# Performance work log

Hardware: AMD Instinct MI355X
Metric: run time of the kernel (lower is better)

Reference implementation:

```python
import jax, jax.numpy as jnp
import numpy as np
import math

B, S, D = 4, 2048, 1024

def setup_inputs() -> dict:
    key = jax.random.key(0)
    ks = jax.random.split(key, 8)
    scale = 1.0 / math.sqrt(D)
    x = jax.random.normal(ks[0], (B, S, D), dtype=jnp.float32)
    # additive causal mask: 0 on/below diag, -1e9 above (broadcast over batch)
    causal = jnp.where(jnp.tril(jnp.ones((S, S), dtype=bool)), 0.0, -1e9).astype(jnp.float32)
    mask = jnp.broadcast_to(causal, (B, S, S))
    Wq = jax.random.uniform(ks[1], (D, D), jnp.float32, -scale, scale)
    bq = jax.random.uniform(ks[2], (D,), jnp.float32, -scale, scale)
    Wk = jax.random.uniform(ks[3], (D, D), jnp.float32, -scale, scale)
    bk = jax.random.uniform(ks[4], (D,), jnp.float32, -scale, scale)
    Wv = jax.random.uniform(ks[5], (D, D), jnp.float32, -scale, scale)
    bv = jax.random.uniform(ks[6], (D,), jnp.float32, -scale, scale)
    return {"x": x, "mask": mask, "Wq": Wq, "bq": bq, "Wk": Wk, "bk": bk, "Wv": Wv, "bv": bv}

def reference(x, mask, Wq, bq, Wk, bk, Wv, bv):
    q = jnp.einsum('bsd,de->bse', x, Wq) + bq
    k = jnp.einsum('bsd,de->bse', x, Wk) + bk
    v = jnp.einsum('bsd,de->bse', x, Wv) + bv
    scores = jnp.einsum('bqd,bkd->bqk', q, k) / math.sqrt(k.shape[-1])
    attn = jax.nn.softmax(scores + mask, axis=-1)
    return jnp.einsum('bqk,bkd->bqd', attn, v)
```

## Files before the change

kernel.cpp:

```cpp
#include <hip/hip_runtime.h>
#include <hip/hip_bf16.h>
#include <math.h>

typedef short v8s __attribute__((ext_vector_type(8)));
typedef short v4s __attribute__((ext_vector_type(4)));
typedef float v4f __attribute__((ext_vector_type(4)));
typedef unsigned short ushort_t;

__device__ __forceinline__ unsigned short f2bf(float f) {
    unsigned int u = __float_as_uint(f);
    u = (u + 0x7FFFu + ((u >> 16) & 1u)) >> 16;
    return (unsigned short)u;
}

__device__ __forceinline__ void load_lds16(const void* g, void* l) {
    __builtin_amdgcn_global_load_lds((const __attribute__((address_space(1))) void*)g,
                                     (__attribute__((address_space(3))) void*)l,
                                     16, 0, 0);
}

#define FENCE() asm volatile("" ::: "memory")
#define BAR() do { FENCE(); __builtin_amdgcn_s_barrier(); FENCE(); } while (0)

__global__ __launch_bounds__(256) void cvt_kernel(const float4* __restrict__ in,
                                                  ushort_t* __restrict__ out, int n4) {
    int i = blockIdx.x * 256 + threadIdx.x;
    int stride = gridDim.x * 256;
    for (; i < n4; i += stride) {
        float4 v = in[i];
        v4s p;
        p[0] = (short)f2bf(v.x); p[1] = (short)f2bf(v.y);
        p[2] = (short)f2bf(v.z); p[3] = (short)f2bf(v.w);
        *(v4s*)(out + (size_t)i * 4) = p;
    }
}

__global__ void transpose_w(const float* __restrict__ W0, const float* __restrict__ W1,
                            const float* __restrict__ W2, ushort_t* __restrict__ WtAll) {
    const float* W = (blockIdx.z == 0) ? W0 : (blockIdx.z == 1 ? W1 : W2);
    ushort_t* out = WtAll + (size_t)blockIdx.z * 1024 * 1024;
    __shared__ float tile[32][33];
    int n0 = blockIdx.x * 32, k0 = blockIdx.y * 32;
    int tx = threadIdx.x, ty = threadIdx.y;
    #pragma unroll
    for (int i = 0; i < 32; i += 8)
        tile[ty + i][tx] = W[(size_t)(k0 + ty + i) * 1024 + n0 + tx];
    __syncthreads();
    #pragma unroll
    for (int i = 0; i < 32; i += 8)
        out[(size_t)(n0 + ty + i) * 1024 + k0 + tx] = f2bf(tile[tx][ty + i]);
}

template <int MODE>
__global__ __launch_bounds__(MODE == 3 ? 256 : 512)
void gemm_ring(const ushort_t* __restrict__ A, int lda, long long strideA,
               const ushort_t* __restrict__ Bt, int ldb, long long strideB,
               const float* __restrict__ bq, const float* __restrict__ bk,
               const float* __restrict__ bv,
               ushort_t* __restrict__ Qb, ushort_t* __restrict__ Kb,
               ushort_t* __restrict__ Vt,
               float* __restrict__ Cf, int ldc, long long strideC, int K)
{
    constexpr int THREADS = (MODE == 3) ? 256 : 512;
    constexpr int BN      = (MODE == 3) ? 128 : 256;
    constexpr int NW      = THREADS / 64;
    constexpr int RPL     = THREADS / 4;
    constexpr int ALINES  = 128 / RPL;
    constexpr int BLINES  = BN / RPL;

    int bx, by, bz = 0;
    int f = blockIdx.x;
    if constexpr (MODE == 0) {
        int xcd = f & 7, i = f >> 3;
        by = xcd * 8 + i / 12;
        bx = i % 12;
    } else if constexpr (MODE == 2) {
        int swz = (f & 7) * 36 + (f >> 3);
        bz = swz / 72; int t = swz % 72;
        int r = 0, c = 0;
        while (c + (r / 2 + 1) <= t) { c += r / 2 + 1; ++r; }
        by = r; bx = t - c;
    } else {
        int swz = (f & 7) * 64 + (f >> 3);
        bz = swz >> 7; int rem = swz & 127;
        by = 15 - (rem >> 3); bx = rem & 7;
    }

    const int tid = threadIdx.x;
    const int lane = tid & 63, wid = tid >> 6;
    const int wm = (NW == 8) ? (wid >> 2) : (wid >> 1);
    const int wc = wid & ((NW == 8) ? 3 : 1);

    const ushort_t* Ab = A + (size_t)bz * strideA;
    const ushort_t* Bb = Bt + (size_t)bz * strideB;

    __shared__ ushort_t As[3][128 * 32];
    __shared__ ushort_t Bs[3][BN * 32];

    const int brow = by * 128, bcol = bx * BN;

    int kEnd = K;
    if constexpr (MODE == 3) { int lim = (by + 1) * 128; kEnd = lim < K ? lim : K; }
    const int nt = kEnd / 32;

    v4f acc[4][4];
    #pragma unroll
    for (int mi = 0; mi < 4; ++mi)
        #pragma unroll
        for (int ni = 0; ni < 4; ++ni)
            acc[mi][ni] = (v4f)0.f;

    const int rr = tid >> 2, slot = tid & 3;
    auto STAGE = [&](int buf, int t) {
        const int k0 = t * 32;
        #pragma unroll
        for (int c = 0; c < ALINES; ++c) {
            int r = c * RPL + rr;
            int sc = ((slot ^ ((r >> 1) & 3)) << 3);
            load_lds16(Ab + (size_t)(brow + r) * lda + k0 + sc,
                       &As[buf][(size_t)(c * RPL + wid * 16) * 32]);
        }
        #pragma unroll
        for (int c = 0; c < BLINES; ++c) {
            int r = c * RPL + rr;
            int sc = ((slot ^ ((r >> 1) & 3)) << 3);
            load_lds16(Bb + (size_t)(bcol + r) * ldb + k0 + sc,
                       &Bs[buf][(size_t)(c * RPL + wid * 16) * 32]);
        }
    };

    const int frow = lane & 15, fq4 = lane >> 4;
    const int csw = ((fq4 ^ ((frow >> 1) & 3)) << 3);

    STAGE(0, 0);
    if (nt > 1) STAGE(1, 1);

    int cur = 0;
    for (int t = 0; t < nt; ++t) {
        if (t + 2 < nt) {
            int tgt = cur ? cur - 1 : 2;
            STAGE(tgt, t + 2);
            if constexpr (MODE == 3) asm volatile("s_waitcnt vmcnt(8)" ::: "memory");
            else                     asm volatile("s_waitcnt vmcnt(6)" ::: "memory");
        } else if (t + 1 < nt) {
            if constexpr (MODE == 3) asm volatile("s_waitcnt vmcnt(4)" ::: "memory");
            else                     asm volatile("s_waitcnt vmcnt(3)" ::: "memory");
        } else {
            asm volatile("s_waitcnt vmcnt(0)" ::: "memory");
        }
        BAR();
        const ushort_t* Ac = &As[cur][0];
        const ushort_t* Bc = &Bs[cur][0];
        v8s a[4], b[4];
        #pragma unroll
        for (int mi = 0; mi < 4; ++mi)
            a[mi] = *(const v8s*)(Ac + (size_t)(wm * 64 + mi * 16 + frow) * 32 + csw);
        #pragma unroll
        for (int ni = 0; ni < 4; ++ni)
            b[ni] = *(const v8s*)(Bc + (size_t)(wc * 64 + ni * 16 + frow) * 32 + csw);
        __builtin_amdgcn_s_setprio(1);
        #pragma unroll
        for (int mi = 0; mi < 4; ++mi)
            #pragma unroll
            for (int ni = 0; ni < 4; ++ni)
                acc[mi][ni] = __builtin_amdgcn_mfma_f32_16x16x32_bf16(a[mi], b[ni], acc[mi][ni], 0, 0, 0);
        __builtin_amdgcn_s_setprio(0);
        BAR();
        cur = (cur == 2) ? 0 : cur + 1;
    }

    const int fr = lane & 15;
    const int fq = lane >> 4;

    if constexpr (MODE == 0) {
        const int route = bx >> 2;
        const int cbase = (bx & 3) * 256 + wc * 64;
        if (route < 2) {
            ushort_t* C = route ? Kb : Qb;
            const float* bias = route ? bk : bq;
            const float scale = route ? 1.0f : 0.03125f;
            #pragma unroll
            for (int ni = 0; ni < 4; ++ni) {
                int cg = cbase + ni * 16 + fr;
                float bb = bias[cg];
                #pragma unroll
                for (int mi = 0; mi < 4; ++mi) {
                    int gr0 = brow + wm * 64 + mi * 16 + fq * 4;
                    #pragma unroll
                    for (int j = 0; j < 4; ++j)
                        C[(size_t)(gr0 + j) * 1024 + cg] = f2bf((acc[mi][ni][j] + bb) * scale);
                }
            }
        } else {
            #pragma unroll
            for (int ni = 0; ni < 4; ++ni) {
                int e = cbase + ni * 16 + fr;
                float bb = bv[e];
                #pragma unroll
                for (int mi = 0; mi < 4; ++mi) {
                    int gr0 = brow + wm * 64 + mi * 16 + fq * 4;
                    int bbat = gr0 >> 11;
                    int sl2 = gr0 & 2047;
                    alignas(8) ushort_t tmp[4];
                    #pragma unroll
                    for (int j = 0; j < 4; ++j)
                        tmp[j] = f2bf(acc[mi][ni][j] + bb);
                    *(v4s*)(Vt + (size_t)bbat * (1024 * 2048) + (size_t)e * 2048 + sl2) =
                        *(const v4s*)tmp;
                }
            }
        }
    } else {
        float* C = Cf + (size_t)bz * strideC;
        #pragma unroll
        for (int ni = 0; ni < 4; ++ni) {
            int gc = bcol + wc * 64 + ni * 16 + fr;
            #pragma unroll
            for (int mi = 0; mi < 4; ++mi) {
                int gr0 = brow + wm * 64 + mi * 16 + fq * 4;
                #pragma unroll
                for (int j = 0; j < 4; ++j)
                    C[(size_t)(gr0 + j) * ldc + gc] = acc[mi][ni][j];
            }
        }
    }
}

__global__ __launch_bounds__(256) void softmax_causal(float* __restrict__ Sc) {
    int row = blockIdx.x;
    int b = row >> 11, i = row & 2047;
    float* srow = Sc + ((size_t)b * 2048 + i) * 2048;
    const int L = i + 1;
    const int Lw = ((i >> 7) + 1) << 7;
    __shared__ float vals[2048];
    __shared__ float red[8];
    int tid = threadIdx.x, lane = tid & 63, wid = tid >> 6;

    float mx = -3.0e38f;
    const int L4 = L >> 2;
    for (int j = tid; j < L4; j += 256) {
        float4 v = ((const float4*)srow)[j];
        ((float4*)vals)[j] = v;
        mx = fmaxf(fmaxf(mx, fmaxf(v.x, v.y)), fmaxf(v.z, v.w));
    }
    {
        int j = (L4 << 2) + tid;
        if (j < L) { float v = srow[j]; vals[j] = v; mx = fmaxf(mx, v); }
    }
    #pragma unroll
    for (int o = 32; o; o >>= 1) mx = fmaxf(mx, __shfl_down(mx, o));
    if (lane == 0) red[wid] = mx;
    __syncthreads();
    mx = fmaxf(fmaxf(red[0], red[1]), fmaxf(red[2], red[3]));

    float sum = 0.f;
    for (int j = tid; j < L; j += 256) {
        float e = __expf(vals[j] - mx);
        vals[j] = e;
        sum += e;
    }
    #pragma unroll
    for (int o = 32; o; o >>= 1) sum += __shfl_down(sum, o);
    if (lane == 0) red[wid + 4] = sum;
    __syncthreads();
    float inv = 1.f / (red[4] + red[5] + red[6] + red[7]);

    ushort_t* prow = (ushort_t*)srow;
    for (int j4 = tid; j4 * 4 < Lw; j4 += 256) {
        int j = j4 * 4;
        float4 v = ((const float4*)vals)[j4];
        v4s p;
        p[0] = (short)f2bf((j     < L) ? v.x * inv : 0.f);
        p[1] = (short)f2bf((j + 1 < L) ? v.y * inv : 0.f);
        p[2] = (short)f2bf((j + 2 < L) ? v.z * inv : 0.f);
        p[3] = (short)f2bf((j + 3 < L) ? v.w * inv : 0.f);
        *(v4s*)(prow + j) = p;
    }
}

extern "C" void kernel_launch(void* const* d_in, const int* in_sizes, int n_in,
                              void* d_out, int out_size, void* d_ws, size_t ws_size,
                              hipStream_t stream) {
    const float* x  = (const float*)d_in[0];
    const float* Wq = (const float*)d_in[2];
    const float* bq = (const float*)d_in[3];
    const float* Wk = (const float*)d_in[4];
    const float* bk = (const float*)d_in[5];
    const float* Wv = (const float*)d_in[6];
    const float* bv = (const float*)d_in[7];

    ushort_t* xb = (ushort_t*)d_ws;
    ushort_t* Wt = xb + (size_t)8192 * 1024;
    ushort_t* Qb = Wt + (size_t)3 * 1024 * 1024;
    ushort_t* Kb = Qb + (size_t)8192 * 1024;
    ushort_t* Vt = Kb + (size_t)8192 * 1024;
    float*    Sc = (float*)(Vt + (size_t)8192 * 1024);

    cvt_kernel<<<2048, 256, 0, stream>>>((const float4*)x, xb, 8192 * 1024 / 4);
    transpose_w<<<dim3(32, 32, 3), dim3(32, 8), 0, stream>>>(Wq, Wk, Wv, Wt);

    gemm_ring<0><<<768, 512, 0, stream>>>(xb, 1024, 0, Wt, 1024, 0,
                                          bq, bk, bv, Qb, Kb, Vt,
                                          nullptr, 0, 0, 1024);

    gemm_ring<2><<<288, 512, 0, stream>>>(Qb, 1024, 2048LL * 1024,
                                          Kb, 1024, 2048LL * 1024,
                                          nullptr, nullptr, nullptr,
                                          nullptr, nullptr, nullptr,
                                          Sc, 2048, 2048LL * 2048, 1024);

    softmax_causal<<<8192, 256, 0, stream>>>(Sc);

    gemm_ring<3><<<512, 256, 0, stream>>>((const ushort_t*)Sc, 4096, 2048LL * 4096,
                                          Vt, 2048, 2048LL * 1024,
                                          nullptr, nullptr, nullptr,
                                          nullptr, nullptr, nullptr,
                                          (float*)d_out, 1024, 2048LL * 1024, 2048);
    (void)in_sizes; (void)n_in; (void)out_size; (void)ws_size;
}
```

Baseline: 176.3 us.

## Store attention scores as fp16 and unify GEMMs on 128x128 tiles

The QK^T GEMM now writes its scores as fp16 instead of fp32. Softmax reads them back as halves and overwrites the same buffer in place with bf16 probabilities, so the P·V GEMM reads a 2048-stride matrix rather than a 4096-stride one. This halves the traffic for the score matrix in both the write and the read. All GEMMs now share a single 256-thread 128x128 tile kernel, which doubles the block counts for the projection and score GEMMs; the triangular tile decode now uses a sqrt estimate. The trade-offs are fp16 range and precision limits on the scores, and smaller tiles with less data reuse in the projection GEMM.

```diff
diff --git a/kernel.cpp b/kernel.cpp
--- a/kernel.cpp
+++ b/kernel.cpp
@@ -1,5 +1,6 @@
 #include <hip/hip_runtime.h>
 #include <hip/hip_bf16.h>
+#include <hip/hip_fp16.h>
 #include <math.h>
 
 typedef short v8s __attribute__((ext_vector_type(8)));
@@ -11,6 +12,14 @@
     unsigned int u = __float_as_uint(f);
     u = (u + 0x7FFFu + ((u >> 16) & 1u)) >> 16;
     return (unsigned short)u;
+}
+__device__ __forceinline__ unsigned short f2h(float f) {
+    __half h = __float2half(f);
+    return *reinterpret_cast<unsigned short*>(&h);
+}
+__device__ __forceinline__ float h2f(unsigned short u) {
+    __half h = *reinterpret_cast<__half*>(&u);
+    return __half2float(h);
 }
 
 __device__ __forceinline__ void load_lds16(const void* g, void* l) {
@@ -52,34 +61,28 @@
 }
 
 template <int MODE>
-__global__ __launch_bounds__(MODE == 3 ? 256 : 512)
-void gemm_ring(const ushort_t* __restrict__ A, int lda, long long strideA,
-               const ushort_t* __restrict__ Bt, int ldb, long long strideB,
-               const float* __restrict__ bq, const float* __restrict__ bk,
-               const float* __restrict__ bv,
-               ushort_t* __restrict__ Qb, ushort_t* __restrict__ Kb,
-               ushort_t* __restrict__ Vt,
-               float* __restrict__ Cf, int ldc, long long strideC, int K)
+__global__ __launch_bounds__(256)
+void gemm128(const ushort_t* __restrict__ A, int lda, long long strideA,
+             const ushort_t* __restrict__ Bt, int ldb, long long strideB,
+             const float* __restrict__ bq, const float* __restrict__ bk,
+             const float* __restrict__ bv,
+             ushort_t* __restrict__ Qb, ushort_t* __restrict__ Kb,
+             ushort_t* __restrict__ Vt,
+             void* __restrict__ Cv, int ldc, long long strideC, int K)
 {
-    constexpr int THREADS = (MODE == 3) ? 256 : 512;
-    constexpr int BN      = (MODE == 3) ? 128 : 256;
-    constexpr int NW      = THREADS / 64;
-    constexpr int RPL     = THREADS / 4;
-    constexpr int ALINES  = 128 / RPL;
-    constexpr int BLINES  = BN / RPL;
-
     int bx, by, bz = 0;
     int f = blockIdx.x;
     if constexpr (MODE == 0) {
-        int xcd = f & 7, i = f >> 3;
-        by = xcd * 8 + i / 12;
-        bx = i % 12;
+        int xcd = f & 7, j = f >> 3;
+        by = xcd * 8 + j / 24;
+        bx = j % 24;
     } else if constexpr (MODE == 2) {
-        int swz = (f & 7) * 36 + (f >> 3);
-        bz = swz / 72; int t = swz % 72;
-        int r = 0, c = 0;
-        while (c + (r / 2 + 1) <= t) { c += r / 2 + 1; ++r; }
-        by = r; bx = t - c;
+        int swz = (f & 7) * 68 + (f >> 3);
+        bz = swz / 136; int t = swz % 136;
+        int r = (int)((sqrtf(8.f * (float)t + 1.f) - 1.f) * 0.5f);
+        while ((r + 1) * (r + 2) / 2 <= t) ++r;
+        while (r * (r + 1) / 2 > t) --r;
+        by = r; bx = t - r * (r + 1) / 2;
     } else {
         int swz = (f & 7) * 64 + (f >> 3);
         bz = swz >> 7; int rem = swz & 127;
@@ -88,16 +91,15 @@
 
     const int tid = threadIdx.x;
     const int lane = tid & 63, wid = tid >> 6;
-    const int wm = (NW == 8) ? (wid >> 2) : (wid >> 1);
-    const int wc = wid & ((NW == 8) ? 3 : 1);
+    const int wm = wid >> 1, wc = wid & 1;
 
     const ushort_t* Ab = A + (size_t)bz * strideA;
     const ushort_t* Bb = Bt + (size_t)bz * strideB;
 
     __shared__ ushort_t As[3][128 * 32];
-    __shared__ ushort_t Bs[3][BN * 32];
-
-    const int brow = by * 128, bcol = bx * BN;
+    __shared__ ushort_t Bs[3][128 * 32];
+
+    const int brow = by * 128, bcol = bx * 128;
 
     int kEnd = K;
     if constexpr (MODE == 3) { int lim = (by + 1) * 128; kEnd = lim < K ? lim : K; }
@@ -114,23 +116,22 @@
     auto STAGE = [&](int buf, int t) {
         const int k0 = t * 32;
         #pragma unroll
-        for (int c = 0; c < ALINES; ++c) {
-            int r = c * RPL + rr;
+        for (int c = 0; c < 2; ++c) {
+            int r = c * 64 + rr;
             int sc = ((slot ^ ((r >> 1) & 3)) << 3);
             load_lds16(Ab + (size_t)(brow + r) * lda + k0 + sc,
-                       &As[buf][(size_t)(c * RPL + wid * 16) * 32]);
-        }
-        #pragma unroll
-        for (int c = 0; c < BLINES; ++c) {
-            int r = c * RPL + rr;
+                       &As[buf][(c * 64 + wid * 16) * 32]);
+        }
+        #pragma unroll
+        for (int c = 0; c < 2; ++c) {
+            int r = c * 64 + rr;
             int sc = ((slot ^ ((r >> 1) & 3)) << 3);
             load_lds16(Bb + (size_t)(bcol + r) * ldb + k0 + sc,
-                       &Bs[buf][(size_t)(c * RPL + wid * 16) * 32]);
+                       &Bs[buf][(c * 64 + wid * 16) * 32]);
         }
     };
 
     const int frow = lane & 15, fq4 = lane >> 4;
-    const int csw = ((fq4 ^ ((frow >> 1) & 3)) << 3);
 
     STAGE(0, 0);
     if (nt > 1) STAGE(1, 1);
@@ -140,11 +141,9 @@
         if (t + 2 < nt) {
             int tgt = cur ? cur - 1 : 2;
             STAGE(tgt, t + 2);
-            if constexpr (MODE == 3) asm volatile("s_waitcnt vmcnt(8)" ::: "memory");
-            else                     asm volatile("s_waitcnt vmcnt(6)" ::: "memory");
+            asm volatile("s_waitcnt vmcnt(8)" ::: "memory");
         } else if (t + 1 < nt) {
-            if constexpr (MODE == 3) asm volatile("s_waitcnt vmcnt(4)" ::: "memory");
-            else                     asm volatile("s_waitcnt vmcnt(3)" ::: "memory");
+            asm volatile("s_waitcnt vmcnt(4)" ::: "memory");
         } else {
             asm volatile("s_waitcnt vmcnt(0)" ::: "memory");
         }
@@ -153,11 +152,15 @@
         const ushort_t* Bc = &Bs[cur][0];
         v8s a[4], b[4];
         #pragma unroll
-        for (int mi = 0; mi < 4; ++mi)
-            a[mi] = *(const v8s*)(Ac + (size_t)(wm * 64 + mi * 16 + frow) * 32 + csw);
-        #pragma unroll
-        for (int ni = 0; ni < 4; ++ni)
-            b[ni] = *(const v8s*)(Bc + (size_t)(wc * 64 + ni * 16 + frow) * 32 + csw);
+        for (int mi = 0; mi < 4; ++mi) {
+            int r = wm * 64 + mi * 16 + frow;
+            a[mi] = *(const v8s*)(Ac + r * 32 + ((fq4 ^ ((r >> 1) & 3)) << 3));
+        }
+        #pragma unroll
+        for (int ni = 0; ni < 4; ++ni) {
+            int r = wc * 64 + ni * 16 + frow;
+            b[ni] = *(const v8s*)(Bc + r * 32 + ((fq4 ^ ((r >> 1) & 3)) << 3));
+        }
         __builtin_amdgcn_s_setprio(1);
         #pragma unroll
         for (int mi = 0; mi < 4; ++mi)
@@ -173,8 +176,8 @@
     const int fq = lane >> 4;
 
     if constexpr (MODE == 0) {
-        const int route = bx >> 2;
-        const int cbase = (bx & 3) * 256 + wc * 64;
+        const int route = bx >> 3;
+        const int cbase = (bx & 7) * 128 + wc * 64;
         if (route < 2) {
             ushort_t* C = route ? Kb : Qb;
             const float* bias = route ? bk : bq;
@@ -210,8 +213,21 @@
                 }
             }
         }
+    } else if constexpr (MODE == 2) {
+        ushort_t* C = (ushort_t*)Cv + (size_t)bz * strideC;
+        #pragma unroll
+        for (int ni = 0; ni < 4; ++ni) {
+            int gc = bcol + wc * 64 + ni * 16 + fr;
+            #pragma unroll
+            for (int mi = 0; mi < 4; ++mi) {
+                int gr0 = brow + wm * 64 + mi * 16 + fq * 4;
+                #pragma unroll
+                for (int j = 0; j < 4; ++j)
+                    C[(size_t)(gr0 + j) * ldc + gc] = f2h(acc[mi][ni][j]);
+            }
+        }
     } else {
-        float* C = Cf + (size_t)bz * strideC;
+        float* C = (float*)Cv + (size_t)bz * strideC;
         #pragma unroll
         for (int ni = 0; ni < 4; ++ni) {
             int gc = bcol + wc * 64 + ni * 16 + fr;
@@ -226,10 +242,10 @@
     }
 }
 
-__global__ __launch_bounds__(256) void softmax_causal(float* __restrict__ Sc) {
+__global__ __launch_bounds__(256) void softmax_causal(ushort_t* __restrict__ Sc) {
     int row = blockIdx.x;
     int b = row >> 11, i = row & 2047;
-    float* srow = Sc + ((size_t)b * 2048 + i) * 2048;
+    ushort_t* srow = Sc + ((size_t)b * 2048 + i) * 2048;
     const int L = i + 1;
     const int Lw = ((i >> 7) + 1) << 7;
     __shared__ float vals[2048];
@@ -238,14 +254,17 @@
 
     float mx = -3.0e38f;
     const int L4 = L >> 2;
-    for (int j = tid; j < L4; j += 256) {
-        float4 v = ((const float4*)srow)[j];
-        ((float4*)vals)[j] = v;
+    for (int j4 = tid; j4 < L4; j4 += 256) {
+        v4s u = *(const v4s*)(srow + j4 * 4);
+        float4 v;
+        v.x = h2f((unsigned short)u[0]); v.y = h2f((unsigned short)u[1]);
+        v.z = h2f((unsigned short)u[2]); v.w = h2f((unsigned short)u[3]);
+        ((float4*)vals)[j4] = v;
         mx = fmaxf(fmaxf(mx, fmaxf(v.x, v.y)), fmaxf(v.z, v.w));
     }
     {
         int j = (L4 << 2) + tid;
-        if (j < L) { float v = srow[j]; vals[j] = v; mx = fmaxf(mx, v); }
+        if (j < L) { float v = h2f(srow[j]); vals[j] = v; mx = fmaxf(mx, v); }
     }
     #pragma unroll
     for (int o = 32; o; o >>= 1) mx = fmaxf(mx, __shfl_down(mx, o));
@@ -265,7 +284,6 @@
     __syncthreads();
     float inv = 1.f / (red[4] + red[5] + red[6] + red[7]);
 
-    ushort_t* prow = (ushort_t*)srow;
     for (int j4 = tid; j4 * 4 < Lw; j4 += 256) {
         int j = j4 * 4;
         float4 v = ((const float4*)vals)[j4];
@@ -274,7 +292,7 @@
         p[1] = (short)f2bf((j + 1 < L) ? v.y * inv : 0.f);
         p[2] = (short)f2bf((j + 2 < L) ? v.z * inv : 0.f);
         p[3] = (short)f2bf((j + 3 < L) ? v.w * inv : 0.f);
-        *(v4s*)(prow + j) = p;
+        *(v4s*)(srow + j) = p;
     }
 }
 
@@ -294,27 +312,27 @@
     ushort_t* Qb = Wt + (size_t)3 * 1024 * 1024;
     ushort_t* Kb = Qb + (size_t)8192 * 1024;
     ushort_t* Vt = Kb + (size_t)8192 * 1024;
-    float*    Sc = (float*)(Vt + (size_t)8192 * 1024);
+    ushort_t* Sc = Vt + (size_t)8192 * 1024;
 
     cvt_kernel<<<2048, 256, 0, stream>>>((const float4*)x, xb, 8192 * 1024 / 4);
     transpose_w<<<dim3(32, 32, 3), dim3(32, 8), 0, stream>>>(Wq, Wk, Wv, Wt);
 
-    gemm_ring<0><<<768, 512, 0, stream>>>(xb, 1024, 0, Wt, 1024, 0,
-                                          bq, bk, bv, Qb, Kb, Vt,
-                                          nullptr, 0, 0, 1024);
-
-    gemm_ring<2><<<288, 512, 0, stream>>>(Qb, 1024, 2048LL * 1024,
-                                          Kb, 1024, 2048LL * 1024,
-                                          nullptr, nullptr, nullptr,
-                                          nullptr, nullptr, nullptr,
-                                          Sc, 2048, 2048LL * 2048, 1024);
+    gemm128<0><<<1536, 256, 0, stream>>>(xb, 1024, 0, Wt, 1024, 0,
+                                         bq, bk, bv, Qb, Kb, Vt,
+                                         nullptr, 0, 0, 1024);
+
+    gemm128<2><<<544, 256, 0, stream>>>(Qb, 1024, 2048LL * 1024,
+                                        Kb, 1024, 2048LL * 1024,
+                                        nullptr, nullptr, nullptr,
+                                        nullptr, nullptr, nullptr,
+                                        Sc, 2048, 2048LL * 2048, 1024);
 
     softmax_causal<<<8192, 256, 0, stream>>>(Sc);
 
-    gemm_ring<3><<<512, 256, 0, stream>>>((const ushort_t*)Sc, 4096, 2048LL * 4096,
-                                          Vt, 2048, 2048LL * 1024,
-                                          nullptr, nullptr, nullptr,
-                                          nullptr, nullptr, nullptr,
-                                          (float*)d_out, 1024, 2048LL * 1024, 2048);
+    gemm128<3><<<512, 256, 0, stream>>>(Sc, 2048, 2048LL * 2048,
+                                        Vt, 2048, 2048LL * 1024,
+                                        nullptr, nullptr, nullptr,
+                                        nullptr, nullptr, nullptr,
+                                        d_out, 1024, 2048LL * 1024, 2048);
     (void)in_sizes; (void)n_in; (void)out_size; (void)ws_size;
 }
```

Measured after the change: 182.1 us. +3.3%, slower.

## Store attention scores as fp16 and restructure GEMM ring pipeline to one barrier

Applied to the files above, without the earlier changes.

The QK^T GEMM now writes scores as fp16 instead of fp32. This halves the score matrix traffic written by the GEMM and read by softmax, and softmax writes bf16 probabilities in place into the same compact buffer. Separately, the GEMM main loop waits and barriers once at the top and then issues the next prefetch, dropping the trailing barrier per iteration. Scores in fp16 could overflow or lose precision for large logits, and the single-barrier ring relies on the three-buffer rotation to avoid overwriting a stage still being read.

```diff
diff --git a/kernel.cpp b/kernel.cpp
--- a/kernel.cpp
+++ b/kernel.cpp
@@ -1,5 +1,6 @@
 #include <hip/hip_runtime.h>
 #include <hip/hip_bf16.h>
+#include <hip/hip_fp16.h>
 #include <math.h>
 
 typedef short v8s __attribute__((ext_vector_type(8)));
@@ -11,6 +12,14 @@
     unsigned int u = __float_as_uint(f);
     u = (u + 0x7FFFu + ((u >> 16) & 1u)) >> 16;
     return (unsigned short)u;
+}
+__device__ __forceinline__ unsigned short f2h(float f) {
+    __half h = __float2half(f);
+    return *reinterpret_cast<unsigned short*>(&h);
+}
+__device__ __forceinline__ float h2f(unsigned short u) {
+    __half h = *reinterpret_cast<__half*>(&u);
+    return __half2float(h);
 }
 
 __device__ __forceinline__ void load_lds16(const void* g, void* l) {
@@ -59,7 +68,7 @@
                const float* __restrict__ bv,
                ushort_t* __restrict__ Qb, ushort_t* __restrict__ Kb,
                ushort_t* __restrict__ Vt,
-               float* __restrict__ Cf, int ldc, long long strideC, int K)
+               void* __restrict__ Cv, int ldc, long long strideC, int K)
 {
     constexpr int THREADS = (MODE == 3) ? 256 : 512;
     constexpr int BN      = (MODE == 3) ? 128 : 256;
@@ -67,6 +76,7 @@
     constexpr int RPL     = THREADS / 4;
     constexpr int ALINES  = 128 / RPL;
     constexpr int BLINES  = BN / RPL;
+    constexpr int LOADS   = ALINES + BLINES;
 
     int bx, by, bz = 0;
     int f = blockIdx.x;
@@ -137,18 +147,16 @@
 
     int cur = 0;
     for (int t = 0; t < nt; ++t) {
+        if (t + 1 < nt) {
+            asm volatile("s_waitcnt vmcnt(%0)" :: "i"(LOADS) : "memory");
+        } else {
+            asm volatile("s_waitcnt vmcnt(0)" ::: "memory");
+        }
+        BAR();
         if (t + 2 < nt) {
             int tgt = cur ? cur - 1 : 2;
             STAGE(tgt, t + 2);
-            if constexpr (MODE == 3) asm volatile("s_waitcnt vmcnt(8)" ::: "memory");
-            else                     asm volatile("s_waitcnt vmcnt(6)" ::: "memory");
-        } else if (t + 1 < nt) {
-            if constexpr (MODE == 3) asm volatile("s_waitcnt vmcnt(4)" ::: "memory");
-            else                     asm volatile("s_waitcnt vmcnt(3)" ::: "memory");
-        } else {
-            asm volatile("s_waitcnt vmcnt(0)" ::: "memory");
-        }
-        BAR();
+        }
         const ushort_t* Ac = &As[cur][0];
         const ushort_t* Bc = &Bs[cur][0];
         v8s a[4], b[4];
@@ -165,7 +173,6 @@
             for (int ni = 0; ni < 4; ++ni)
                 acc[mi][ni] = __builtin_amdgcn_mfma_f32_16x16x32_bf16(a[mi], b[ni], acc[mi][ni], 0, 0, 0);
         __builtin_amdgcn_s_setprio(0);
-        BAR();
         cur = (cur == 2) ? 0 : cur + 1;
     }
 
@@ -210,8 +217,21 @@
                 }
             }
         }
+    } else if constexpr (MODE == 2) {
+        ushort_t* C = (ushort_t*)Cv + (size_t)bz * strideC;
+        #pragma unroll
+        for (int ni = 0; ni < 4; ++ni) {
+            int gc = bcol + wc * 64 + ni * 16 + fr;
+            #pragma unroll
+            for (int mi = 0; mi < 4; ++mi) {
+                int gr0 = brow + wm * 64 + mi * 16 + fq * 4;
+                #pragma unroll
+                for (int j = 0; j < 4; ++j)
+                    C[(size_t)(gr0 + j) * ldc + gc] = f2h(acc[mi][ni][j]);
+            }
+        }
     } else {
-        float* C = Cf + (size_t)bz * strideC;
+        float* C = (float*)Cv + (size_t)bz * strideC;
         #pragma unroll
         for (int ni = 0; ni < 4; ++ni) {
             int gc = bcol + wc * 64 + ni * 16 + fr;
@@ -226,10 +246,10 @@
     }
 }
 
-__global__ __launch_bounds__(256) void softmax_causal(float* __restrict__ Sc) {
+__global__ __launch_bounds__(256) void softmax_causal(ushort_t* __restrict__ Sc) {
     int row = blockIdx.x;
     int b = row >> 11, i = row & 2047;
-    float* srow = Sc + ((size_t)b * 2048 + i) * 2048;
+    ushort_t* srow = Sc + ((size_t)b * 2048 + i) * 2048;
     const int L = i + 1;
     const int Lw = ((i >> 7) + 1) << 7;
     __shared__ float vals[2048];
@@ -238,14 +258,17 @@
 
     float mx = -3.0e38f;
     const int L4 = L >> 2;
-    for (int j = tid; j < L4; j += 256) {
-        float4 v = ((const float4*)srow)[j];
-        ((float4*)vals)[j] = v;
+    for (int j4 = tid; j4 < L4; j4 += 256) {
+        v4s u = *(const v4s*)(srow + j4 * 4);
+        float4 v;
+        v.x = h2f((unsigned short)u[0]); v.y = h2f((unsigned short)u[1]);
+        v.z = h2f((unsigned short)u[2]); v.w = h2f((unsigned short)u[3]);
+        ((float4*)vals)[j4] = v;
         mx = fmaxf(fmaxf(mx, fmaxf(v.x, v.y)), fmaxf(v.z, v.w));
     }
     {
         int j = (L4 << 2) + tid;
-        if (j < L) { float v = srow[j]; vals[j] = v; mx = fmaxf(mx, v); }
+        if (j < L) { float v = h2f(srow[j]); vals[j] = v; mx = fmaxf(mx, v); }
     }
     #pragma unroll
     for (int o = 32; o; o >>= 1) mx = fmaxf(mx, __shfl_down(mx, o));
@@ -265,7 +288,6 @@
     __syncthreads();
     float inv = 1.f / (red[4] + red[5] + red[6] + red[7]);
 
-    ushort_t* prow = (ushort_t*)srow;
     for (int j4 = tid; j4 * 4 < Lw; j4 += 256) {
         int j = j4 * 4;
         float4 v = ((const float4*)vals)[j4];
@@ -274,7 +296,7 @@
         p[1] = (short)f2bf((j + 1 < L) ? v.y * inv : 0.f);
         p[2] = (short)f2bf((j + 2 < L) ? v.z * inv : 0.f);
         p[3] = (short)f2bf((j + 3 < L) ? v.w * inv : 0.f);
-        *(v4s*)(prow + j) = p;
+        *(v4s*)(srow + j) = p;
     }
 }
 
@@ -294,7 +316,7 @@
     ushort_t* Qb = Wt + (size_t)3 * 1024 * 1024;
     ushort_t* Kb = Qb + (size_t)8192 * 1024;
     ushort_t* Vt = Kb + (size_t)8192 * 1024;
-    float*    Sc = (float*)(Vt + (size_t)8192 * 1024);
+    ushort_t* Sc = Vt + (size_t)8192 * 1024;
 
     cvt_kernel<<<2048, 256, 0, stream>>>((const float4*)x, xb, 8192 * 1024 / 4);
     transpose_w<<<dim3(32, 32, 3), dim3(32, 8), 0, stream>>>(Wq, Wk, Wv, Wt);
@@ -311,10 +333,10 @@
 
     softmax_causal<<<8192, 256, 0, stream>>>(Sc);
 
-    gemm_ring<3><<<512, 256, 0, stream>>>((const ushort_t*)Sc, 4096, 2048LL * 4096,
+    gemm_ring<3><<<512, 256, 0, stream>>>(Sc, 2048, 2048LL * 2048,
                                           Vt, 2048, 2048LL * 1024,
                                           nullptr, nullptr, nullptr,
                                           nullptr, nullptr, nullptr,
-                                          (float*)d_out, 1024, 2048LL * 1024, 2048);
+                                          d_out, 1024, 2048LL * 1024, 2048);
     (void)in_sizes; (void)n_in; (void)out_size; (void)ws_size;
 }
```

New measurement: 177.8 us. About the same (+0.9%).
